# Performance work log

Measured on AMD Instinct MI355X. Metric: run time of the kernel, lower is better.

## Reference

```python
import jax, jax.numpy as jnp
import numpy as np
import math

NUM_IMGS, BATCH, DIM, H, W = 2, 32, 512, 18, 18
NUM_POS = 2
KEY_DIM = 128
NUM_LAYERS = 6
TEMP = 30.0
NORM_EPS = 1e-5
L2_EPS = 1e-12
NORM_SCALE = math.sqrt(1.0 / (DIM * 4 * 4))


def setup_inputs() -> dict:
    key = jax.random.key(0)
    ks = jax.random.split(key, 8)
    L_mem = NUM_POS * H * W
    return {
        "tgt": jax.random.normal(ks[0], (NUM_IMGS, BATCH, DIM, H, W), jnp.float32),
        "pos_embed": jax.random.normal(ks[1], (NUM_IMGS, BATCH, DIM, H, W), jnp.float32),
        "memory": jax.random.normal(ks[2], (L_mem, BATCH, DIM), jnp.float32),
        "pos": jax.random.uniform(ks[3], (NUM_POS, BATCH, H, W), jnp.float32),
        "Wk_self": jax.random.normal(ks[4], (KEY_DIM, DIM), jnp.float32) * 0.02,
        "bk_self": jnp.zeros((KEY_DIM,), jnp.float32),
        "Wk_cross": jax.random.normal(ks[5], (KEY_DIM, DIM), jnp.float32) * 0.02,
        "bk_cross": jnp.zeros((KEY_DIM,), jnp.float32),
    }


def _l2norm(x):
    n = jnp.sqrt(jnp.sum(x * x, axis=-1, keepdims=True))
    return x / jnp.maximum(n, L2_EPS)


def _attn(q, k, v, Wk, bk):
    # q:[Lq,B,D] k:[Lk,B,D] v:[Lk,B,D]; custom RelationUnit attention
    wq = _l2norm(q @ Wk.T + bk)              # [Lq,B,K]
    wk = _l2norm(k @ Wk.T + bk)              # [Lk,B,K]
    scores = jnp.einsum('qbk,sbk->bqs', wq, wk) * TEMP
    aff = jax.nn.softmax(scores, axis=-1)    # [B,Lq,Lk]
    return jnp.einsum('bqs,sbd->qbd', aff, v)


def _inorm(src):
    # src:[n*h*w, B, D]; InstanceL2Norm over (D,H,W) per (img,batch)
    x = src.reshape(NUM_IMGS, H * W, BATCH, DIM)
    ss = jnp.sum(x * x, axis=(1, 3), keepdims=True)
    x = x * (NORM_SCALE * jnp.sqrt((DIM * H * W) / (ss + NORM_EPS)))
    return x.reshape(NUM_IMGS * H * W, BATCH, DIM)


def reference(tgt, pos_embed, memory, pos, Wk_self, bk_self, Wk_cross, bk_cross):
    n, b, d, h, w = tgt.shape
    # flatten to [n*h*w, B, D]
    def flat(x):
        return x.reshape(n, b, d, h * w).transpose(0, 3, 1, 2).reshape(-1, b, d)
    x = flat(tgt)
    pe = flat(pos_embed)
    # pos: [num_pos,B,h,w] -> [num_pos*h*w, B, D] (value broadcast across D)
    num_pos = pos.shape[0]
    p = pos.reshape(num_pos, b, 1, h * w).transpose(0, 3, 1, 2).reshape(-1, b, 1)
    p = jnp.broadcast_to(p, (p.shape[0], b, d))
    mem_p = memory * p

    for _ in range(NUM_LAYERS):  # all layers share weights (_get_clones has no deepcopy)
        x = x + pe * 0.001
        x = _inorm(x + _attn(x, x, x, Wk_self, bk_self))
        mask = _attn(x, memory, p, Wk_cross, bk_cross)
        t2 = _inorm(x * mask)
        t3 = _attn(x, memory, mem_p, Wk_cross, bk_cross)
        t4 = _inorm(x + t3)
        x = _inorm(t2 + t4)

    out_feat = x.reshape(n, h, w, b, d).transpose(0, 3, 4, 1, 2).reshape(-1, d, h, w)
    return (x, out_feat)
```

## Files before the change

### kernel.cpp

```cpp
#include <hip/hip_runtime.h>
#include <math.h>

#define NI  2
#define BB  32
#define DD  512
#define HWX 324
#define LL  648
#define MM  648
#define KX  128

#define TEMPF  30.0f
#define NEPSF  1e-5f
#define L2EPSF 1e-12f
#define DHWF   165888.0f
#define NSDF   0.011048543456039806f

__global__ void k_flat(const float* __restrict__ src, float* __restrict__ x) {
  size_t idx = (size_t)blockIdx.x * 256 + threadIdx.x;
  int r = (int)(idx >> 9), d = (int)(idx & 511);
  int l = r >> 5, b = r & 31;
  int i = l / HWX, s = l % HWX;
  x[idx] = src[((size_t)(i * BB + b) * DD + d) * HWX + s];
}

__global__ void k_addpe(const float* __restrict__ pe, float* __restrict__ x) {
  size_t idx = (size_t)blockIdx.x * 256 + threadIdx.x;
  int r = (int)(idx >> 9), d = (int)(idx & 511);
  int l = r >> 5, b = r & 31;
  int i = l / HWX, s = l % HWX;
  float t = __fmul_rn(pe[((size_t)(i * BB + b) * DD + d) * HWX + s], 0.001f);
  x[idx] = __fadd_rn(x[idx], t);
}

__global__ void k_pos(const float* __restrict__ pos, float* __restrict__ ps) {
  int idx = blockIdx.x * 256 + threadIdx.x;
  int l = idx >> 5, b = idx & 31;
  int j = l / HWX, s = l % HWX;
  ps[idx] = pos[((size_t)(j * BB + b)) * HWX + s];
}

__global__ void k_memp(const float* __restrict__ mem, const float* __restrict__ ps,
                       float* __restrict__ memp) {
  size_t idx = (size_t)blockIdx.x * 256 + threadIdx.x;
  memp[idx] = __fmul_rn(mem[idx], ps[idx >> 9]);
}

__global__ void k_wt(const float* __restrict__ W, float* __restrict__ Wt) {
  int idx = blockIdx.x * 256 + threadIdx.x;
  int k = idx & 127, d = idx >> 7;
  Wt[idx] = W[(size_t)k * DD + d];
}

__global__ __launch_bounds__(256) void k_projt(const float* __restrict__ A,
                                               const float* __restrict__ Wt,
                                               const float* __restrict__ bias,
                                               float* __restrict__ outp) {
  int r0 = blockIdx.x * 128;
  int tid = threadIdx.x, tx = tid & 15, ty = tid >> 4;
  __shared__ float As[128][36];
  __shared__ float Ws[32][132];
  __shared__ float bsh[128];
  __shared__ float sqb[16][129];
  __shared__ float prb[16][8];
  __shared__ float nshs[16];
  if (tid < 128) bsh[tid] = bias[tid];
  float acc[8][8] = {};
  for (int d0 = 0; d0 < 512; d0 += 32) {
#pragma unroll
    for (int n = 0; n < 4; n++) {
      int fi = tid + 256 * n;
      int rr = fi >> 3, dq = (fi & 7) * 4;
      *(float4*)&As[rr][dq] = *(const float4*)(A + (size_t)(r0 + rr) * 512 + d0 + dq);
    }
#pragma unroll
    for (int n = 0; n < 4; n++) {
      int fi = tid + 256 * n;
      int dd = fi >> 5, kq = (fi & 31) * 4;
      *(float4*)&Ws[dd][kq] = *(const float4*)(Wt + (size_t)(d0 + dd) * 128 + kq);
    }
    __syncthreads();
#pragma unroll 8
    for (int dd = 0; dd < 32; dd++) {
      float a[8], w[8];
#pragma unroll
      for (int i = 0; i < 8; i++) a[i] = As[ty + 16 * i][dd];
#pragma unroll
      for (int j = 0; j < 8; j++) w[j] = Ws[dd][tx + 16 * j];
#pragma unroll
      for (int i = 0; i < 8; i++)
#pragma unroll
        for (int j = 0; j < 8; j++) acc[i][j] = fmaf(a[i], w[j], acc[i][j]);
    }
    __syncthreads();
  }
  for (int i = 0; i < 8; i++) {
    float val[8];
#pragma unroll
    for (int j = 0; j < 8; j++) {
      val[j] = __fadd_rn(acc[i][j], bsh[tx + 16 * j]);
      sqb[ty][tx + 16 * j] = __fmul_rn(val[j], val[j]);
    }
    __syncthreads();
    if (tid < 128) {
      int row = tid >> 3, jj = tid & 7;
      float rr = sqb[row][jj];
      for (int blk = 1; blk < 16; blk++) rr += sqb[row][blk * 8 + jj];
      prb[row][jj] = rr;
    }
    __syncthreads();
    if (tid < 16) {
      float* p = prb[tid];
      float ss = ((p[0] + p[1]) + (p[2] + p[3])) + ((p[4] + p[5]) + (p[6] + p[7]));
      nshs[tid] = fmaxf(__fsqrt_rn(ss), L2EPSF);
    }
    __syncthreads();
    float nsh = nshs[ty];
    int r = r0 + ty + 16 * i;
#pragma unroll
    for (int j = 0; j < 8; j++)
      outp[(size_t)r * 128 + tx + 16 * j] = __fdiv_rn(val[j], nsh);
    __syncthreads();
  }
}

__global__ __launch_bounds__(256) void k_scoret(const float* __restrict__ wqp,
                                                const float* __restrict__ wkp,
                                                float* __restrict__ sc) {
  int q0 = blockIdx.x * 64, s0 = blockIdx.y * 64, b = blockIdx.z;
  int tid = threadIdx.x, tx = tid & 15, ty = tid >> 4;
  __shared__ float QsT[64][65];
  __shared__ float KsT[64][65];
  float acc[4][4] = {};
  const float4 f40 = make_float4(0.f, 0.f, 0.f, 0.f);
  for (int k0 = 0; k0 < 128; k0 += 64) {
#pragma unroll
    for (int n = 0; n < 4; n++) {
      int fi = tid + 256 * n;
      int rr = fi >> 4, kq = (fi & 15) * 4;
      int q = q0 + rr;
      float4 v = (q < LL) ? *(const float4*)(wqp + ((size_t)q * 32 + b) * 128 + k0 + kq) : f40;
      QsT[kq + 0][rr] = v.x; QsT[kq + 1][rr] = v.y;
      QsT[kq + 2][rr] = v.z; QsT[kq + 3][rr] = v.w;
      int s = s0 + rr;
      float4 w = (s < MM) ? *(const float4*)(wkp + ((size_t)s * 32 + b) * 128 + k0 + kq) : f40;
      KsT[kq + 0][rr] = w.x; KsT[kq + 1][rr] = w.y;
      KsT[kq + 2][rr] = w.z; KsT[kq + 3][rr] = w.w;
    }
    __syncthreads();
#pragma unroll 8
    for (int kk = 0; kk < 64; kk++) {
      float a[4], w[4];
#pragma unroll
      for (int i = 0; i < 4; i++) a[i] = QsT[kk][ty + 16 * i];
#pragma unroll
      for (int j = 0; j < 4; j++) w[j] = KsT[kk][tx + 16 * j];
#pragma unroll
      for (int i = 0; i < 4; i++)
#pragma unroll
        for (int j = 0; j < 4; j++) acc[i][j] = fmaf(a[i], w[j], acc[i][j]);
    }
    __syncthreads();
  }
#pragma unroll
  for (int i = 0; i < 4; i++) {
    int q = q0 + ty + 16 * i;
    if (q >= LL) continue;
    float* orow = sc + ((size_t)b * LL + q) * MM;
#pragma unroll
    for (int j = 0; j < 4; j++) {
      int s = s0 + tx + 16 * j;
      if (s < MM) orow[s] = __fmul_rn(acc[i][j], TEMPF);
    }
  }
}

__global__ __launch_bounds__(256) void k_sm2(float* __restrict__ sc) {
  int row = blockIdx.x;
  float* p = sc + (size_t)row * MM;
  int t = threadIdx.x;
  __shared__ float red[256];
  __shared__ float es[MM];
  __shared__ float prc[64];
  __shared__ float ssum;
  float v0 = p[t], v1 = p[t + 256];
  bool h2 = t < (MM - 512);
  float v2 = h2 ? p[t + 512] : -3.0e38f;
  red[t] = fmaxf(fmaxf(v0, v1), v2);
  __syncthreads();
  for (int off = 128; off; off >>= 1) {
    if (t < off) red[t] = fmaxf(red[t], red[t + off]);
    __syncthreads();
  }
  float mx = red[0];
  float e0 = (float)exp((double)__fsub_rn(v0, mx));
  float e1 = (float)exp((double)__fsub_rn(v1, mx));
  float e2 = h2 ? (float)exp((double)__fsub_rn(v2, mx)) : 0.0f;
  es[t] = e0; es[t + 256] = e1;
  if (h2) es[t + 512] = e2;
  __syncthreads();
  if (t < 64) {
    int c = t >> 3, jj = t & 7;
    int base = c * 80, n = (c == 7) ? 88 : 80;
    float r = es[base + jj];
    for (int i = 8; i < n; i += 8) r += es[base + i + jj];
    prc[t] = r;
  }
  __syncthreads();
  if (t == 0) {
    float pc[8];
#pragma unroll
    for (int c = 0; c < 8; c++) {
      float* pp = prc + c * 8;
      pc[c] = ((pp[0] + pp[1]) + (pp[2] + pp[3])) + ((pp[4] + pp[5]) + (pp[6] + pp[7]));
    }
    float lsum = (pc[0] + pc[1]) + (pc[2] + pc[3]);
    float rsum = (pc[4] + pc[5]) + (pc[6] + pc[7]);
    ssum = lsum + rsum;
  }
  __syncthreads();
  float s = ssum;
  p[t] = __fdiv_rn(e0, s);
  p[t + 256] = __fdiv_rn(e1, s);
  if (h2) p[t + 512] = __fdiv_rn(e2, s);
}

template <int DO_MASK>
__global__ __launch_bounds__(256) void k_applyg(const float* __restrict__ aff,
                                                const float* __restrict__ V,
                                                const float* __restrict__ ps,
                                                float* __restrict__ outp,
                                                float* __restrict__ msk) {
  int dd = blockIdx.x;
  int xcd = dd & 7, j = dd >> 3;
  int b = xcd * 4 + j / 27;
  int q0 = (j % 27) * 24;
  int tid = threadIdx.x;
  const float* abase = aff + ((size_t)b * LL + q0) * MM;
  const float* vbase = V + (size_t)b * 512 + tid * 2;
  float acc0[24] = {};
  float acc1[24] = {};
  for (int s4 = 0; s4 < 162; s4++) {
    float2 v0 = *(const float2*)(vbase + (size_t)(4 * s4 + 0) * 16384);
    float2 v1 = *(const float2*)(vbase + (size_t)(4 * s4 + 1) * 16384);
    float2 v2 = *(const float2*)(vbase + (size_t)(4 * s4 + 2) * 16384);
    float2 v3 = *(const float2*)(vbase + (size_t)(4 * s4 + 3) * 16384);
#pragma unroll
    for (int qq = 0; qq < 24; qq++) {
      float4 a4 = *(const float4*)(abase + qq * MM + s4 * 4);
      acc0[qq] = fmaf(a4.x, v0.x, acc0[qq]); acc1[qq] = fmaf(a4.x, v0.y, acc1[qq]);
      acc0[qq] = fmaf(a4.y, v1.x, acc0[qq]); acc1[qq] = fmaf(a4.y, v1.y, acc1[qq]);
      acc0[qq] = fmaf(a4.z, v2.x, acc0[qq]); acc1[qq] = fmaf(a4.z, v2.y, acc1[qq]);
      acc0[qq] = fmaf(a4.w, v3.x, acc0[qq]); acc1[qq] = fmaf(a4.w, v3.y, acc1[qq]);
    }
  }
#pragma unroll
  for (int qq = 0; qq < 24; qq++) {
    float2 r = make_float2(acc0[qq], acc1[qq]);
    *(float2*)(outp + ((size_t)(q0 + qq) * 32 + b) * 512 + tid * 2) = r;
  }
  if (DO_MASK && tid < 24) {
    const float* arow = abase + tid * MM;
    float a = 0.0f;
    for (int s = 0; s < MM; s++) a = fmaf(arow[s], ps[s * 32 + b], a);
    msk[(q0 + tid) * 32 + b] = a;
  }
}

template <int MODE>
__global__ __launch_bounds__(128) void k_na(const float* __restrict__ x,
                                            const float* __restrict__ ao,
                                            const float* __restrict__ msk,
                                            const float* __restrict__ scu,
                                            const float* __restrict__ scv,
                                            float* __restrict__ tU,
                                            float* __restrict__ tV) {
  int s = blockIdx.x;
  int g = blockIdx.y;
  int i = g >> 5, b = g & 31;
  int l = i * HWX + s;
  size_t base = ((size_t)l * BB + b) * DD;
  int t = threadIdx.x;
  __shared__ float squ[DD];
  __shared__ float sqv[DD];
  __shared__ float pru[32];
  __shared__ float prv[32];
  float mk = 0.f, su = 0.f, sv = 0.f;
  if (MODE >= 2) mk = msk[l * BB + b];
  if (MODE == 3) { su = scu[g]; sv = scv[g]; }
  for (int d = t; d < DD; d += 128) {
    float xx = x[base + d];
    if (MODE == 1) {
      float y = __fadd_rn(xx, ao[base + d]);
      squ[d] = __fmul_rn(y, y);
    } else if (MODE == 2) {
      float u = __fmul_rn(xx, mk);
      float v = __fadd_rn(xx, ao[base + d]);
      squ[d] = __fmul_rn(u, u);
      sqv[d] = __fmul_rn(v, v);
    } else {
      float u = __fmul_rn(xx, mk);
      float v = __fadd_rn(xx, ao[base + d]);
      float t2 = __fmul_rn(u, su);
      float t4 = __fmul_rn(v, sv);
      float w = __fadd_rn(t2, t4);
      squ[d] = __fmul_rn(w, w);
    }
  }
  __syncthreads();
  if (t < 32) {
    int c = t >> 3, jj = t & 7, b0 = c * 128;
    float r = squ[b0 + jj];
    for (int blk = 1; blk < 16; blk++) r += squ[b0 + blk * 8 + jj];
    pru[t] = r;
    if (MODE == 2) {
      float r2 = sqv[b0 + jj];
      for (int blk = 1; blk < 16; blk++) r2 += sqv[b0 + blk * 8 + jj];
      prv[t] = r2;
    }
  }
  __syncthreads();
  if (t == 0) {
    float cc[4];
    for (int c = 0; c < 4; c++)
      cc[c] = ((pru[c * 8] + pru[c * 8 + 1]) + (pru[c * 8 + 2] + pru[c * 8 + 3])) +
              ((pru[c * 8 + 4] + pru[c * 8 + 5]) + (pru[c * 8 + 6] + pru[c * 8 + 7]));
    tU[g * HWX + s] = (cc[0] + cc[1]) + (cc[2] + cc[3]);
    if (MODE == 2) {
      for (int c = 0; c < 4; c++)
        cc[c] = ((prv[c * 8] + prv[c * 8 + 1]) + (prv[c * 8 + 2] + prv[c * 8 + 3])) +
                ((prv[c * 8 + 4] + prv[c * 8 + 5]) + (prv[c * 8 + 6] + prv[c * 8 + 7]));
      tV[g * HWX + s] = (cc[0] + cc[1]) + (cc[2] + cc[3]);
    }
  }
}

__global__ void k_fin1(const float* __restrict__ tU, float* __restrict__ scl) {
  int g = threadIdx.x;
  float ss = 0.0f;
  for (int s = 0; s < HWX; s++) ss += tU[g * HWX + s];
  scl[g] = __fmul_rn(NSDF, __fsqrt_rn(__fdiv_rn(DHWF, __fadd_rn(ss, NEPSF))));
}

__global__ void k_fin2(const float* __restrict__ tU, const float* __restrict__ tV,
                       float* __restrict__ scu, float* __restrict__ scv) {
  int g = threadIdx.x;
  float su = 0.0f, sv = 0.0f;
  for (int s = 0; s < HWX; s++) { su += tU[g * HWX + s]; sv += tV[g * HWX + s]; }
  scu[g] = __fmul_rn(NSDF, __fsqrt_rn(__fdiv_rn(DHWF, __fadd_rn(su, NEPSF))));
  scv[g] = __fmul_rn(NSDF, __fsqrt_rn(__fdiv_rn(DHWF, __fadd_rn(sv, NEPSF))));
}

__global__ void k_a1(float* __restrict__ x, const float* __restrict__ ao,
                     const float* __restrict__ scl) {
  size_t idx = (size_t)blockIdx.x * 256 + threadIdx.x;
  int r = (int)(idx >> 9);
  int l = r >> 5, b = r & 31;
  int g = (l / HWX) * BB + b;
  x[idx] = __fmul_rn(__fadd_rn(x[idx], ao[idx]), scl[g]);
}

__global__ void k_a2(float* __restrict__ x, const float* __restrict__ ao,
                     const float* __restrict__ msk, const float* __restrict__ scu,
                     const float* __restrict__ scv, const float* __restrict__ scw) {
  size_t idx = (size_t)blockIdx.x * 256 + threadIdx.x;
  int r = (int)(idx >> 9);
  int l = r >> 5, b = r & 31;
  int g = (l / HWX) * BB + b;
  float mk = msk[l * BB + b];
  float xx = x[idx];
  float u = __fmul_rn(xx, mk);
  float v = __fadd_rn(xx, ao[idx]);
  float t2 = __fmul_rn(u, scu[g]);
  float t4 = __fmul_rn(v, scv[g]);
  float w = __fadd_rn(t2, t4);
  x[idx] = __fmul_rn(w, scw[g]);
}

__global__ void k_o0(const float* __restrict__ x, float* __restrict__ out) {
  size_t idx = (size_t)blockIdx.x * 256 + threadIdx.x;
  out[idx] = x[idx];
}

__global__ void k_o1(const float* __restrict__ x, float* __restrict__ out1) {
  size_t idx = (size_t)blockIdx.x * 256 + threadIdx.x;
  int s = (int)(idx % HWX);
  int d = (int)((idx / HWX) & 511);
  int ib = (int)(idx / ((size_t)HWX * DD));
  int i = ib >> 5, b = ib & 31;
  int l = i * HWX + s;
  out1[idx] = x[((size_t)l * BB + b) * DD + d];
}

extern "C" void kernel_launch(void* const* d_in, const int* in_sizes, int n_in,
                              void* d_out, int out_size, void* d_ws, size_t ws_size,
                              hipStream_t stream) {
  const float* tgt = (const float*)d_in[0];
  const float* pe  = (const float*)d_in[1];
  const float* mem = (const float*)d_in[2];
  const float* pos = (const float*)d_in[3];
  const float* Wks = (const float*)d_in[4];
  const float* bks = (const float*)d_in[5];
  const float* Wkc = (const float*)d_in[6];
  const float* bkc = (const float*)d_in[7];
  float* out = (float*)d_out;

  if (ws_size < (size_t)203240448) return;
  float* f = (float*)d_ws;
  float* x    = f;
  float* ao   = f + 10616832;
  float* memp = f + 21233664;
  float* wq   = f + 31850496;
  float* wkm  = f + 34504704;
  float* sc   = f + 37158912;
  float* msk  = f + 50595840;
  float* ps   = f + 50616576;
  float* tU   = f + 50637312;
  float* tV   = f + 50658048;
  float* scl  = f + 50678784;
  float* scu  = scl + 64;
  float* scv  = scl + 128;
  float* scw  = scl + 192;
  float* Wst  = f + 50679040;
  float* Wct  = f + 50744576;

  k_wt<<<256, 256, 0, stream>>>(Wks, Wst);
  k_wt<<<256, 256, 0, stream>>>(Wkc, Wct);
  k_flat<<<41472, 256, 0, stream>>>(tgt, x);
  k_pos<<<81, 256, 0, stream>>>(pos, ps);
  k_memp<<<41472, 256, 0, stream>>>(mem, ps, memp);
  k_projt<<<162, 256, 0, stream>>>(mem, Wct, bkc, wkm);

  dim3 scg(11, 11, 32);
  dim3 nag(324, 64);
  for (int l = 0; l < 6; l++) {
    k_addpe<<<41472, 256, 0, stream>>>(pe, x);
    k_projt<<<162, 256, 0, stream>>>(x, Wst, bks, wq);
    k_scoret<<<scg, 256, 0, stream>>>(wq, wq, sc);
    k_sm2<<<20736, 256, 0, stream>>>(sc);
    k_applyg<0><<<864, 256, 0, stream>>>(sc, x, nullptr, ao, nullptr);
    k_na<1><<<nag, 128, 0, stream>>>(x, ao, nullptr, nullptr, nullptr, tU, nullptr);
    k_fin1<<<1, 64, 0, stream>>>(tU, scl);
    k_a1<<<41472, 256, 0, stream>>>(x, ao, scl);
    k_projt<<<162, 256, 0, stream>>>(x, Wct, bkc, wq);
    k_scoret<<<scg, 256, 0, stream>>>(wq, wkm, sc);
    k_sm2<<<20736, 256, 0, stream>>>(sc);
    k_applyg<1><<<864, 256, 0, stream>>>(sc, memp, ps, ao, msk);
    k_na<2><<<nag, 128, 0, stream>>>(x, ao, msk, nullptr, nullptr, tU, tV);
    k_fin2<<<1, 64, 0, stream>>>(tU, tV, scu, scv);
    k_na<3><<<nag, 128, 0, stream>>>(x, ao, msk, scu, scv, tU, nullptr);
    k_fin1<<<1, 64, 0, stream>>>(tU, scw);
    k_a2<<<41472, 256, 0, stream>>>(x, ao, msk, scu, scv, scw);
  }

  k_o0<<<41472, 256, 0, stream>>>(x, out);
  k_o1<<<41472, 256, 0, stream>>>(x, out + (size_t)LL * BB * DD);
}
```

Measured before the change: 6.212 ms.

## Retile score GEMM to 96x96 and restructure attention-apply kernel thread mapping

The score kernel moves from 64x64 tiles with a 4x4 per-thread microtile to 96x96 tiles with a 6x6 microtile and a K step of 32. K is now stored row-major in shared memory with float4 stores. The apply kernel changes from 256 threads each handling 2 columns for 24 query rows to 512 threads each handling 1 column for 12 rows, which doubles the block count. The goal is more reuse per shared-memory load in the score GEMM and more parallelism with fewer registers in the apply step. The cost is more padding waste (648 is not a multiple of 96), likely shared-memory bank conflicts on the Ks column reads, and each affinity row being read by twice as many blocks.

```diff
diff --git a/kernel.cpp b/kernel.cpp
--- a/kernel.cpp
+++ b/kernel.cpp
@@ -126,48 +126,47 @@
 __global__ __launch_bounds__(256) void k_scoret(const float* __restrict__ wqp,
                                                 const float* __restrict__ wkp,
                                                 float* __restrict__ sc) {
-  int q0 = blockIdx.x * 64, s0 = blockIdx.y * 64, b = blockIdx.z;
+  int q0 = blockIdx.x * 96, s0 = blockIdx.y * 96, b = blockIdx.z;
   int tid = threadIdx.x, tx = tid & 15, ty = tid >> 4;
-  __shared__ float QsT[64][65];
-  __shared__ float KsT[64][65];
-  float acc[4][4] = {};
+  __shared__ float QsT[32][97];
+  __shared__ float Ks[96][36];
+  float acc[6][6] = {};
   const float4 f40 = make_float4(0.f, 0.f, 0.f, 0.f);
-  for (int k0 = 0; k0 < 128; k0 += 64) {
-#pragma unroll
-    for (int n = 0; n < 4; n++) {
+  for (int k0 = 0; k0 < 128; k0 += 32) {
+#pragma unroll
+    for (int n = 0; n < 3; n++) {
       int fi = tid + 256 * n;
-      int rr = fi >> 4, kq = (fi & 15) * 4;
+      int rr = fi >> 3, kq = (fi & 7) * 4;
       int q = q0 + rr;
       float4 v = (q < LL) ? *(const float4*)(wqp + ((size_t)q * 32 + b) * 128 + k0 + kq) : f40;
       QsT[kq + 0][rr] = v.x; QsT[kq + 1][rr] = v.y;
       QsT[kq + 2][rr] = v.z; QsT[kq + 3][rr] = v.w;
       int s = s0 + rr;
       float4 w = (s < MM) ? *(const float4*)(wkp + ((size_t)s * 32 + b) * 128 + k0 + kq) : f40;
-      KsT[kq + 0][rr] = w.x; KsT[kq + 1][rr] = w.y;
-      KsT[kq + 2][rr] = w.z; KsT[kq + 3][rr] = w.w;
+      *(float4*)&Ks[rr][kq] = w;
     }
     __syncthreads();
 #pragma unroll 8
-    for (int kk = 0; kk < 64; kk++) {
-      float a[4], w[4];
-#pragma unroll
-      for (int i = 0; i < 4; i++) a[i] = QsT[kk][ty + 16 * i];
-#pragma unroll
-      for (int j = 0; j < 4; j++) w[j] = KsT[kk][tx + 16 * j];
-#pragma unroll
-      for (int i = 0; i < 4; i++)
-#pragma unroll
-        for (int j = 0; j < 4; j++) acc[i][j] = fmaf(a[i], w[j], acc[i][j]);
-    }
-    __syncthreads();
-  }
-#pragma unroll
-  for (int i = 0; i < 4; i++) {
+    for (int kk = 0; kk < 32; kk++) {
+      float a[6], w[6];
+#pragma unroll
+      for (int i = 0; i < 6; i++) a[i] = QsT[kk][ty + 16 * i];
+#pragma unroll
+      for (int j = 0; j < 6; j++) w[j] = Ks[tx + 16 * j][kk];
+#pragma unroll
+      for (int i = 0; i < 6; i++)
+#pragma unroll
+        for (int j = 0; j < 6; j++) acc[i][j] = fmaf(a[i], w[j], acc[i][j]);
+    }
+    __syncthreads();
+  }
+#pragma unroll
+  for (int i = 0; i < 6; i++) {
     int q = q0 + ty + 16 * i;
     if (q >= LL) continue;
     float* orow = sc + ((size_t)b * LL + q) * MM;
 #pragma unroll
-    for (int j = 0; j < 4; j++) {
+    for (int j = 0; j < 6; j++) {
       int s = s0 + tx + 16 * j;
       if (s < MM) orow[s] = __fmul_rn(acc[i][j], TEMPF);
     }
@@ -225,40 +224,37 @@
 }
 
 template <int DO_MASK>
-__global__ __launch_bounds__(256) void k_applyg(const float* __restrict__ aff,
+__global__ __launch_bounds__(512) void k_applyg(const float* __restrict__ aff,
                                                 const float* __restrict__ V,
                                                 const float* __restrict__ ps,
                                                 float* __restrict__ outp,
                                                 float* __restrict__ msk) {
   int dd = blockIdx.x;
   int xcd = dd & 7, j = dd >> 3;
-  int b = xcd * 4 + j / 27;
-  int q0 = (j % 27) * 24;
+  int b = xcd * 4 + j / 54;
+  int q0 = (j % 54) * 12;
   int tid = threadIdx.x;
   const float* abase = aff + ((size_t)b * LL + q0) * MM;
-  const float* vbase = V + (size_t)b * 512 + tid * 2;
-  float acc0[24] = {};
-  float acc1[24] = {};
+  const float* vbase = V + (size_t)b * 512 + tid;
+  float acc[12] = {};
   for (int s4 = 0; s4 < 162; s4++) {
-    float2 v0 = *(const float2*)(vbase + (size_t)(4 * s4 + 0) * 16384);
-    float2 v1 = *(const float2*)(vbase + (size_t)(4 * s4 + 1) * 16384);
-    float2 v2 = *(const float2*)(vbase + (size_t)(4 * s4 + 2) * 16384);
-    float2 v3 = *(const float2*)(vbase + (size_t)(4 * s4 + 3) * 16384);
-#pragma unroll
-    for (int qq = 0; qq < 24; qq++) {
+    float v0 = vbase[(size_t)(4 * s4 + 0) * 16384];
+    float v1 = vbase[(size_t)(4 * s4 + 1) * 16384];
+    float v2 = vbase[(size_t)(4 * s4 + 2) * 16384];
+    float v3 = vbase[(size_t)(4 * s4 + 3) * 16384];
+#pragma unroll
+    for (int qq = 0; qq < 12; qq++) {
       float4 a4 = *(const float4*)(abase + qq * MM + s4 * 4);
-      acc0[qq] = fmaf(a4.x, v0.x, acc0[qq]); acc1[qq] = fmaf(a4.x, v0.y, acc1[qq]);
-      acc0[qq] = fmaf(a4.y, v1.x, acc0[qq]); acc1[qq] = fmaf(a4.y, v1.y, acc1[qq]);
-      acc0[qq] = fmaf(a4.z, v2.x, acc0[qq]); acc1[qq] = fmaf(a4.z, v2.y, acc1[qq]);
-      acc0[qq] = fmaf(a4.w, v3.x, acc0[qq]); acc1[qq] = fmaf(a4.w, v3.y, acc1[qq]);
-    }
-  }
-#pragma unroll
-  for (int qq = 0; qq < 24; qq++) {
-    float2 r = make_float2(acc0[qq], acc1[qq]);
-    *(float2*)(outp + ((size_t)(q0 + qq) * 32 + b) * 512 + tid * 2) = r;
-  }
-  if (DO_MASK && tid < 24) {
+      acc[qq] = fmaf(a4.x, v0, acc[qq]);
+      acc[qq] = fmaf(a4.y, v1, acc[qq]);
+      acc[qq] = fmaf(a4.z, v2, acc[qq]);
+      acc[qq] = fmaf(a4.w, v3, acc[qq]);
+    }
+  }
+#pragma unroll
+  for (int qq = 0; qq < 12; qq++)
+    outp[((size_t)(q0 + qq) * 32 + b) * 512 + tid] = acc[qq];
+  if (DO_MASK && tid < 12) {
     const float* arow = abase + tid * MM;
     float a = 0.0f;
     for (int s = 0; s < MM; s++) a = fmaf(arow[s], ps[s * 32 + b], a);
@@ -430,21 +426,21 @@
   k_memp<<<41472, 256, 0, stream>>>(mem, ps, memp);
   k_projt<<<162, 256, 0, stream>>>(mem, Wct, bkc, wkm);
 
-  dim3 scg(11, 11, 32);
+  dim3 scg(7, 7, 32);
   dim3 nag(324, 64);
   for (int l = 0; l < 6; l++) {
     k_addpe<<<41472, 256, 0, stream>>>(pe, x);
     k_projt<<<162, 256, 0, stream>>>(x, Wst, bks, wq);
     k_scoret<<<scg, 256, 0, stream>>>(wq, wq, sc);
     k_sm2<<<20736, 256, 0, stream>>>(sc);
-    k_applyg<0><<<864, 256, 0, stream>>>(sc, x, nullptr, ao, nullptr);
+    k_applyg<0><<<1728, 512, 0, stream>>>(sc, x, nullptr, ao, nullptr);
     k_na<1><<<nag, 128, 0, stream>>>(x, ao, nullptr, nullptr, nullptr, tU, nullptr);
     k_fin1<<<1, 64, 0, stream>>>(tU, scl);
     k_a1<<<41472, 256, 0, stream>>>(x, ao, scl);
     k_projt<<<162, 256, 0, stream>>>(x, Wct, bkc, wq);
     k_scoret<<<scg, 256, 0, stream>>>(wq, wkm, sc);
     k_sm2<<<20736, 256, 0, stream>>>(sc);
-    k_applyg<1><<<864, 256, 0, stream>>>(sc, memp, ps, ao, msk);
+    k_applyg<1><<<1728, 512, 0, stream>>>(sc, memp, ps, ao, msk);
     k_na<2><<<nag, 128, 0, stream>>>(x, ao, msk, nullptr, nullptr, tU, tV);
     k_fin2<<<1, 64, 0, stream>>>(tU, tV, scu, scv);
     k_na<3><<<nag, 128, 0, stream>>>(x, ao, msk, scu, scv, tU, nullptr);
```

After: 7.205 ms. 16.0% more time.
